# Kernel optimization log

Measured on AMD Instinct MI355X. Metric: run time of the kernel, lower is better.

Reference implementation:

```python
import jax, jax.numpy as jnp
import numpy as np
from math import ceil

CAPACITY_FACTOR = 2.0
MIN_CAPACITY = 4


def setup_inputs() -> dict:
    key = jax.random.key(0)
    ks = jax.random.split(key, 4)
    B, S, D, Di, E = 4, 2048, 1024, 4096, 8
    x = jax.random.normal(ks[0], (B, S, D), dtype=jnp.float32)
    Wr = jax.random.normal(ks[1], (D, E), dtype=jnp.float32) * (D ** -0.5)
    W1 = jax.random.normal(ks[2], (E, D, Di), dtype=jnp.float32) * (D ** -0.5)
    b1 = jnp.zeros((E, Di), dtype=jnp.float32)
    W2 = jax.random.normal(ks[3], (E, Di, D), dtype=jnp.float32) * (Di ** -0.5)
    b2 = jnp.zeros((E, D), dtype=jnp.float32)
    return {"x": x, "Wr": Wr, "W1": W1, "b1": b1, "W2": W2, "b2": b2}


def reference(x, Wr, W1, b1, W2, b2):
    B, S, D = x.shape
    E = Wr.shape[1]
    N = B * S
    k = max(MIN_CAPACITY, ceil(N * CAPACITY_FACTOR / E))  # expert capacity (static)

    xt = x.reshape(N, D)
    scores = jax.nn.softmax(xt @ Wr, axis=-1)          # [N, E] router probs
    G, idx = jax.lax.top_k(scores.T, k)                 # [E, k]: each expert picks top-k tokens

    # dispatch: equivalent to P @ x with P = one_hot(idx, N)
    X_in = xt[idx]                                      # [E, k, D]

    # per-expert MLP (batched over experts): Linear -> GELU(exact) -> Linear
    h = jax.nn.gelu(jnp.einsum('ekd,edh->ekh', X_in, W1) + b1[:, None, :], approximate=False)
    X_e = jnp.einsum('ekh,ehd->ekd', h, W2) + b2[:, None, :]  # [E, k, D]

    # combine: einsum('ijl,ij,ijd->ld', P, G, X_e) == scatter-add of G*X_e at idx
    contrib = (G[..., None] * X_e).reshape(E * k, D)
    out = jnp.zeros((N, D), dtype=x.dtype).at[idx.reshape(-1)].add(contrib)
    return out.reshape(B, S, D)
```

## Files before the change

### kernel.cpp

```cpp
#include <hip/hip_runtime.h>
#include <hip/hip_bf16.h>
#include <cstdint>
#include <cstddef>

#define NTOK 8192
#define DMODEL 1024
#define DFF 4096
#define NEXP 8
#define CAP 2048

typedef __attribute__((ext_vector_type(8))) __bf16 bf16x8;
typedef __attribute__((ext_vector_type(4))) float f32x4;

__device__ __forceinline__ void gload16(const void* g, void* l) {
  __builtin_amdgcn_global_load_lds(
      (__attribute__((address_space(1))) void*)(g),
      (__attribute__((address_space(3))) void*)(l),
      16, 0, 0);
}
#define VMWAIT_(n) asm volatile("s_waitcnt vmcnt(" #n ")" ::: "memory")
#define VMWAIT(n) VMWAIT_(n)
#define MEMFENCE asm volatile("" ::: "memory")

__global__ __launch_bounds__(256) void zero_f32(float* p, int n4) {
  int i = blockIdx.x * blockDim.x + threadIdx.x;
  int stride = gridDim.x * blockDim.x;
  float4 z = make_float4(0.f, 0.f, 0.f, 0.f);
  for (; i < n4; i += stride) ((float4*)p)[i] = z;
}

__global__ __launch_bounds__(256) void router_kernel(
    const float* __restrict__ x, const float* __restrict__ Wr,
    float* __restrict__ scoresT, __hip_bfloat16* __restrict__ xb) {
  const int lane = threadIdx.x & 63;
  const int t = blockIdx.x * 4 + (threadIdx.x >> 6);
  const float* xr = x + (size_t)t * DMODEL;
  float acc[NEXP];
#pragma unroll
  for (int j = 0; j < NEXP; ++j) acc[j] = 0.f;
#pragma unroll
  for (int it = 0; it < DMODEL / 64; ++it) {
    int d = it * 64 + lane;
    float xv = xr[d];
    xb[(size_t)t * DMODEL + d] = __float2bfloat16(xv);
    const float4* w = (const float4*)(Wr + (size_t)d * NEXP);
    float4 w0 = w[0], w1 = w[1];
    acc[0] += xv * w0.x; acc[1] += xv * w0.y; acc[2] += xv * w0.z; acc[3] += xv * w0.w;
    acc[4] += xv * w1.x; acc[5] += xv * w1.y; acc[6] += xv * w1.z; acc[7] += xv * w1.w;
  }
#pragma unroll
  for (int off = 32; off; off >>= 1) {
#pragma unroll
    for (int j = 0; j < NEXP; ++j) acc[j] += __shfl_xor(acc[j], off);
  }
  float m = acc[0];
#pragma unroll
  for (int j = 1; j < NEXP; ++j) m = fmaxf(m, acc[j]);
  float s = 0.f;
#pragma unroll
  for (int j = 0; j < NEXP; ++j) { acc[j] = expf(acc[j] - m); s += acc[j]; }
  float inv = 1.f / s;
  if (lane < NEXP) scoresT[(size_t)lane * NTOK + t] = acc[lane] * inv;
}

__global__ __launch_bounds__(256) void topk_kernel(
    const float* __restrict__ scoresT, float* __restrict__ G, int* __restrict__ IDX) {
  __shared__ uint32_t sb[NTOK];
  __shared__ uint32_t hist[256];
  __shared__ uint32_t s_prefix, s_rem;
  __shared__ uint32_t eq_list[256];
  __shared__ uint32_t eq_cnt, gt_cnt;
  const int e = blockIdx.x, tid = threadIdx.x;
  const float* se = scoresT + (size_t)e * NTOK;
  for (int i = tid; i < NTOK; i += 256) sb[i] = __float_as_uint(se[i]);
  if (tid == 0) { s_prefix = 0u; s_rem = CAP; eq_cnt = 0u; gt_cnt = 0u; }
  __syncthreads();
  for (int r = 0; r < 4; ++r) {
    const int shift = 24 - 8 * r;
    for (int i = tid; i < 256; i += 256) hist[i] = 0u;
    __syncthreads();
    uint32_t pfx = s_prefix;
    for (int i = tid; i < NTOK; i += 256) {
      uint32_t b = sb[i];
      if (((b >> shift) >> 8) == pfx) atomicAdd(&hist[(b >> shift) & 255u], 1u);
    }
    __syncthreads();
    if (tid == 0) {
      uint32_t rem = s_rem, cum = 0u;
      int d = 255;
      for (; d > 0; --d) {
        if (cum + hist[d] >= rem) break;
        cum += hist[d];
      }
      s_prefix = (pfx << 8) | (uint32_t)d;
      s_rem = rem - cum;
    }
    __syncthreads();
  }
  const uint32_t T = s_prefix, need = s_rem;
  for (int i = tid; i < NTOK; i += 256) {
    uint32_t b = sb[i];
    if (b > T) {
      uint32_t p = atomicAdd(&gt_cnt, 1u);
      IDX[(size_t)e * CAP + p] = i;
      G[(size_t)e * CAP + p] = __uint_as_float(b);
    } else if (b == T) {
      uint32_t c = atomicAdd(&eq_cnt, 1u);
      if (c < 256u) eq_list[c] = (uint32_t)i;
    }
  }
  __syncthreads();
  if (tid == 0) {
    uint32_t base = gt_cnt;
    uint32_t c = eq_cnt < 256u ? eq_cnt : 256u;
    for (uint32_t s = 0; s < need; ++s) {
      uint32_t mv = 0xFFFFFFFFu; int mi = 0;
      for (uint32_t j = 0; j < c; ++j)
        if (eq_list[j] < mv) { mv = eq_list[j]; mi = (int)j; }
      eq_list[mi] = 0xFFFFFFFFu;
      IDX[(size_t)e * CAP + base + s] = (int)mv;
      G[(size_t)e * CAP + base + s] = __uint_as_float(T);
    }
  }
}

__global__ __launch_bounds__(256) void transpose_cvt(
    const float* __restrict__ in, __hip_bfloat16* __restrict__ out, int R, int C) {
  __shared__ float tile[32][33];
  const int e = blockIdx.z;
  const float* ine = in + (size_t)e * R * C;
  __hip_bfloat16* oute = out + (size_t)e * R * C;
  const int c0 = blockIdx.x * 32, r0 = blockIdx.y * 32;
  const int tx = threadIdx.x, ty = threadIdx.y;
#pragma unroll
  for (int i = 0; i < 4; ++i)
    tile[ty + i * 8][tx] = ine[(size_t)(r0 + ty + i * 8) * C + (c0 + tx)];
  __syncthreads();
#pragma unroll
  for (int i = 0; i < 4; ++i)
    oute[(size_t)(c0 + ty + i * 8) * R + (r0 + tx)] =
        __float2bfloat16(tile[tx][ty + i * 8]);
}


#define RD_A(BASE, H)                                                          \
  {                                                                            \
    _Pragma("unroll") for (int mi = 0; mi < 4; ++mi)                           \
        _Pragma("unroll") for (int ks = 0; ks < 2; ++ks) av[mi][ks] =          \
        *(const bf16x8*)((BASE) + Ab + offA[(H)*4 + mi][ks]);                  \
  }
#define RD_B(BASE, BV, H2)                                                     \
  {                                                                            \
    _Pragma("unroll") for (int ni = 0; ni < 2; ++ni)                           \
        _Pragma("unroll") for (int ks = 0; ks < 2; ++ks) BV[ni][ks] =          \
        *(const bf16x8*)((BASE) + Bb + offB[(H2)*2 + ni][ks]);                 \
  }
#define STAGE_A(H, BUF)                                                        \
  {                                                                            \
    gload16(pa[(H)*2], (BUF) + (H)*16384 + dst);                               \
    pa[(H)*2] += 128;                                                          \
    gload16(pa[(H)*2 + 1], (BUF) + (H)*16384 + 8192 + dst);                    \
    pa[(H)*2 + 1] += 128;                                                      \
  }
#define STAGE_B(H, BUF)                                                        \
  {                                                                            \
    gload16(pb[(H)*2], (BUF) + 32768 + (H)*16384 + dst);                       \
    pb[(H)*2] += 128;                                                          \
    gload16(pb[(H)*2 + 1], (BUF) + 32768 + (H)*16384 + 8192 + dst);            \
    pb[(H)*2 + 1] += 128;                                                      \
  }
#define PH_PRE                                                                 \
  __builtin_amdgcn_s_barrier();                                                \
  MEMFENCE;                                                                    \
  asm volatile("s_waitcnt lgkmcnt(0)" ::: "memory");                           \
  __builtin_amdgcn_sched_barrier(0);                                           \
  __builtin_amdgcn_s_setprio(1);
#define PH_POST                                                                \
  __builtin_amdgcn_s_setprio(0);                                               \
  __builtin_amdgcn_s_barrier();                                                \
  MEMFENCE;
#define MFMA_Q(MB, NB, BV)                                                     \
  {                                                                            \
    _Pragma("unroll") for (int mi = 0; mi < 4; ++mi)                           \
        _Pragma("unroll") for (int ni = 0; ni < 2; ++ni)                       \
            _Pragma("unroll") for (int ks = 0; ks < 2; ++ks)                   \
                acc[(MB) + mi][(NB) + ni] =                                    \
        __builtin_amdgcn_mfma_f32_16x16x32_bf16(                               \
            av[mi][ks], BV[ni][ks], acc[(MB) + mi][(NB) + ni], 0, 0, 0);       \
  }

template <int NKT>
__device__ __forceinline__ void gemm_core8(
    const char* pa0, const char* pa1, const char* pa2, const char* pa3,
    const char* pb0, const char* pb1, const char* pb2, const char* pb3,
    char* smem, f32x4 (&acc)[8][4]) {
  const int tid = threadIdx.x;
  const int wave = tid >> 6, lane = tid & 63;
  const int wm = wave >> 2, wn = wave & 3;
  const int lrow = lane & 15, lgrp = lane >> 4;
  const int dst = tid * 16;

  const char* pa[4] = {pa0, pa1, pa2, pa3};
  const char* pb[4] = {pb0, pb1, pb2, pb3};

  int offA[8][2], offB[4][2];
#pragma unroll
  for (int mi = 0; mi < 8; ++mi) {
    int rL = mi * 16 + lrow;
#pragma unroll
    for (int ks = 0; ks < 2; ++ks)
      offA[mi][ks] = rL * 128 + ((((ks * 4 + lgrp) + rL) & 7) << 4);
  }
#pragma unroll
  for (int ni = 0; ni < 4; ++ni) {
    int rL = (wn & 1) * 64 + ni * 16 + lrow;
#pragma unroll
    for (int ks = 0; ks < 2; ++ks)
      offB[ni][ks] = rL * 128 + ((((ks * 4 + lgrp) + rL) & 7) << 4);
  }
  const int Ab = wm * 16384;
  const int Bb = 32768 + (wn >> 1) * 16384;

  char* b0 = smem;
  char* b1 = smem + 65536;

#pragma unroll
  for (int g = 0; g < 4; ++g) {
    gload16(pa[g], b0 + (g >> 1) * 16384 + (g & 1) * 8192 + dst);
    pa[g] += 128;
  }
#pragma unroll
  for (int g = 0; g < 4; ++g) {
    gload16(pb[g], b0 + 32768 + (g >> 1) * 16384 + (g & 1) * 8192 + dst);
    pb[g] += 128;
  }
#pragma unroll
  for (int g = 0; g < 4; ++g) {
    gload16(pb[g], b1 + 32768 + (g >> 1) * 16384 + (g & 1) * 8192 + dst);
    pb[g] += 128;
  }
  VMWAIT(4);
  __builtin_amdgcn_s_barrier();
  MEMFENCE;

  bf16x8 av[4][2], bv0[2][2], bv1[2][2];

  for (int i = 0; i < NKT / 2; ++i) {
    const bool st2 = (2 * i + 2 < NKT);
    const bool st3 = (2 * i + 3 < NKT);

    RD_A(b0, 0); RD_B(b0, bv0, 0);
    STAGE_A(0, b1);
    PH_PRE; MFMA_Q(0, 0, bv0); PH_POST;
    RD_B(b0, bv1, 1);
    STAGE_A(1, b1);
    PH_PRE; MFMA_Q(0, 2, bv1); PH_POST;
    RD_A(b0, 1);
    if (st2) STAGE_B(0, b0);
    PH_PRE; MFMA_Q(4, 2, bv1); PH_POST;
    if (st2) STAGE_B(1, b0);
    PH_PRE; MFMA_Q(4, 0, bv0);
    __builtin_amdgcn_s_setprio(0);
    if (st2) { VMWAIT(4); } else { VMWAIT(0); }
    __builtin_amdgcn_s_barrier();
    MEMFENCE;

    RD_A(b1, 0); RD_B(b1, bv0, 0);
    if (st2) STAGE_A(0, b0);
    PH_PRE; MFMA_Q(0, 0, bv0); PH_POST;
    RD_B(b1, bv1, 1);
    if (st2) STAGE_A(1, b0);
    PH_PRE; MFMA_Q(0, 2, bv1); PH_POST;
    RD_A(b1, 1);
    if (st3) STAGE_B(0, b1);
    PH_PRE; MFMA_Q(4, 2, bv1); PH_POST;
    if (st3) STAGE_B(1, b1);
    PH_PRE; MFMA_Q(4, 0, bv0);
    __builtin_amdgcn_s_setprio(0);
    if (st3) { VMWAIT(4); }
    __builtin_amdgcn_s_barrier();
    MEMFENCE;
  }
}

__device__ __forceinline__ float gelu_tanh(float v) {
  float t = 0.7978845608028654f * (v + 0.044715f * v * v * v);
  float e = __expf(2.f * t);
  float th = 1.f - 2.f / (e + 1.f);
  return 0.5f * v * (1.f + th);
}

__global__ __launch_bounds__(512, 2) void gemm1_kernel(
    const __hip_bfloat16* __restrict__ xb,
    const __hip_bfloat16* __restrict__ W1t,
    const float* __restrict__ b1,
    const int* __restrict__ IDX,
    __hip_bfloat16* __restrict__ h, int e0, int nblk) {
  __shared__ __align__(16) char smem[131072];
  int lin = blockIdx.x;
  { int q = nblk >> 3; lin = (lin & 7) * q + (lin >> 3); }
  const int tm = lin & 7, tn = (lin >> 3) & 15, ez = lin >> 7;
  const int e = e0 + ez;
  const int tid = threadIdx.x, wave = tid >> 6, lane = tid & 63;
  const int wm = wave >> 2, wn = wave & 3;
  const int lrow = lane & 15, lgrp = lane >> 4;

  const int r0 = tid >> 3;
  const int ksrc = (((tid & 7) - r0) & 7) * 16;
  const char* pa[4]; const char* pb[4];
#pragma unroll
  for (int g = 0; g < 4; ++g) {
    int m = g * 64 + r0;
    int tok = IDX[e * CAP + tm * 256 + m];
    pa[g] = (const char*)(xb + (size_t)tok * DMODEL) + ksrc;
    int n = g * 64 + r0;
    pb[g] = (const char*)(W1t + ((size_t)e * DFF + tn * 256 + n) * DMODEL) + ksrc;
  }

  f32x4 acc[8][4];
  f32x4 zero = {0.f, 0.f, 0.f, 0.f};
#pragma unroll
  for (int mi = 0; mi < 8; ++mi)
#pragma unroll
    for (int ni = 0; ni < 4; ++ni) acc[mi][ni] = zero;

  gemm_core8<DMODEL / 64>(pa[0], pa[1], pa[2], pa[3],
                          pb[0], pb[1], pb[2], pb[3], smem, acc);

  __hip_bfloat16* he = h + (size_t)ez * CAP * DFF;
  const float* b1e = b1 + (size_t)e * DFF;
  float bvals[4];
#pragma unroll
  for (int ni = 0; ni < 4; ++ni)
    bvals[ni] = b1e[tn * 256 + wn * 64 + ni * 16 + lrow];
#pragma unroll
  for (int mi = 0; mi < 8; ++mi) {
#pragma unroll
    for (int j = 0; j < 4; ++j) {
      int row = tm * 256 + wm * 128 + mi * 16 + lgrp * 4 + j;
      __hip_bfloat16* hrow = he + (size_t)row * DFF;
#pragma unroll
      for (int ni = 0; ni < 4; ++ni) {
        int col = tn * 256 + wn * 64 + ni * 16 + lrow;
        float v = acc[mi][ni][j] + bvals[ni];
        hrow[col] = __float2bfloat16(gelu_tanh(v));
      }
    }
  }
}

__global__ __launch_bounds__(512, 2) void gemm2_kernel(
    const __hip_bfloat16* __restrict__ h,
    const __hip_bfloat16* __restrict__ W2t,
    const float* __restrict__ b2,
    const int* __restrict__ IDX, const float* __restrict__ G,
    float* __restrict__ out, int e0, int nblk) {
  __shared__ __align__(16) char smem[131072];
  int lin = blockIdx.x;
  { int q = nblk >> 3; lin = (lin & 7) * q + (lin >> 3); }
  const int tm = lin & 7, tn = (lin >> 3) & 3, ez = lin >> 5;
  const int e = e0 + ez;
  const int tid = threadIdx.x, wave = tid >> 6, lane = tid & 63;
  const int wm = wave >> 2, wn = wave & 3;
  const int lrow = lane & 15, lgrp = lane >> 4;

  const int r0 = tid >> 3;
  const int ksrc = (((tid & 7) - r0) & 7) * 16;
  const char* pa[4]; const char* pb[4];
#pragma unroll
  for (int g = 0; g < 4; ++g) {
    int m = g * 64 + r0;
    pa[g] = (const char*)(h + ((size_t)ez * CAP + tm * 256 + m) * DFF) + ksrc;
    int n = g * 64 + r0;
    pb[g] = (const char*)(W2t + ((size_t)e * DMODEL + tn * 256 + n) * DFF) + ksrc;
  }

  f32x4 acc[8][4];
  f32x4 zero = {0.f, 0.f, 0.f, 0.f};
#pragma unroll
  for (int mi = 0; mi < 8; ++mi)
#pragma unroll
    for (int ni = 0; ni < 4; ++ni) acc[mi][ni] = zero;

  gemm_core8<DFF / 64>(pa[0], pa[1], pa[2], pa[3],
                       pb[0], pb[1], pb[2], pb[3], smem, acc);

  const float* b2e = b2 + (size_t)e * DMODEL;
  const int* idxe = IDX + (size_t)e * CAP;
  const float* ge = G + (size_t)e * CAP;
  float bvals[4];
#pragma unroll
  for (int ni = 0; ni < 4; ++ni)
    bvals[ni] = b2e[tn * 256 + wn * 64 + ni * 16 + lrow];
#pragma unroll
  for (int mi = 0; mi < 8; ++mi) {
#pragma unroll
    for (int j = 0; j < 4; ++j) {
      int row = tm * 256 + wm * 128 + mi * 16 + lgrp * 4 + j;
      float g = ge[row];
      int tok = idxe[row];
      float* orow = out + (size_t)tok * DMODEL;
#pragma unroll
      for (int ni = 0; ni < 4; ++ni) {
        int col = tn * 256 + wn * 64 + ni * 16 + lrow;
        atomicAdd(orow + col, (acc[mi][ni][j] + bvals[ni]) * g);
      }
    }
  }
}

extern "C" void kernel_launch(void* const* d_in, const int* in_sizes, int n_in,
                              void* d_out, int out_size, void* d_ws, size_t ws_size,
                              hipStream_t stream) {
  const float* x  = (const float*)d_in[0];
  const float* Wr = (const float*)d_in[1];
  const float* W1 = (const float*)d_in[2];
  const float* b1 = (const float*)d_in[3];
  const float* W2 = (const float*)d_in[4];
  const float* b2 = (const float*)d_in[5];
  float* out = (float*)d_out;
  char* ws = (char*)d_ws;

  size_t off = 0;
  float* scoresT = (float*)(ws + off); off += (size_t)NEXP * NTOK * 4;
  float* G       = (float*)(ws + off); off += (size_t)NEXP * CAP * 4;
  int*   IDX     = (int*)(ws + off);   off += (size_t)NEXP * CAP * 4;
  __hip_bfloat16* xb  = (__hip_bfloat16*)(ws + off); off += (size_t)NTOK * DMODEL * 2;
  __hip_bfloat16* W1t = (__hip_bfloat16*)(ws + off); off += (size_t)NEXP * DFF * DMODEL * 2;
  __hip_bfloat16* W2t = (__hip_bfloat16*)(ws + off); off += (size_t)NEXP * DMODEL * DFF * 2;
  __hip_bfloat16* hbuf = (__hip_bfloat16*)(ws + off);
  size_t h_per_e = (size_t)CAP * DFF * 2;
  size_t avail = (ws_size > off) ? (ws_size - off) : 0;
  int EC = (int)(avail / h_per_e);
  if (EC < 1) EC = 1;
  if (EC > NEXP) EC = NEXP;

  zero_f32<<<512, 256, 0, stream>>>(out, out_size / 4);
  router_kernel<<<NTOK / 4, 256, 0, stream>>>(x, Wr, scoresT, xb);
  topk_kernel<<<NEXP, 256, 0, stream>>>(scoresT, G, IDX);
  transpose_cvt<<<dim3(DFF / 32, DMODEL / 32, NEXP), dim3(32, 8), 0, stream>>>(
      W1, W1t, DMODEL, DFF);
  transpose_cvt<<<dim3(DMODEL / 32, DFF / 32, NEXP), dim3(32, 8), 0, stream>>>(
      W2, W2t, DFF, DMODEL);
  for (int e0 = 0; e0 < NEXP; e0 += EC) {
    int ne = (NEXP - e0 < EC) ? (NEXP - e0) : EC;
    int nblk1 = 128 * ne;
    gemm1_kernel<<<nblk1, 512, 0, stream>>>(xb, W1t, b1, IDX, hbuf, e0, nblk1);
    int nblk2 = 32 * ne;
    gemm2_kernel<<<nblk2, 512, 0, stream>>>(hbuf, W2t, b2, IDX, G, out, e0, nblk2);
  }
}
```

Measured before the change: 472.2 us.

## Vectorize stores in transpose and GEMM1 epilogue, drop trailing phase barrier

The weight transpose now writes pairs of bf16 values as 32-bit stores instead of scalar 16-bit stores. The GEMM1 epilogue stages the GELU output tile in swizzled LDS and then writes it out with coalesced 16-byte global stores instead of scattered 2-byte stores. The barrier after each MFMA phase in the pipelined core is removed, leaving only a priority reset. This cuts global store transactions and sync overhead, but removing the barrier risks LDS races if the next stage overwrites buffers that other waves are still reading.

```diff
diff --git a/kernel.cpp b/kernel.cpp
--- a/kernel.cpp
+++ b/kernel.cpp
@@ -136,10 +136,15 @@
   for (int i = 0; i < 4; ++i)
     tile[ty + i * 8][tx] = ine[(size_t)(r0 + ty + i * 8) * C + (c0 + tx)];
   __syncthreads();
-#pragma unroll
-  for (int i = 0; i < 4; ++i)
-    oute[(size_t)(c0 + ty + i * 8) * R + (r0 + tx)] =
-        __float2bfloat16(tile[tx][ty + i * 8]);
+  const int rp = (tx & 15) * 2;
+#pragma unroll
+  for (int i = 0; i < 2; ++i) {
+    int cl = ty + (tx >> 4) * 8 + i * 16;
+    __hip_bfloat16 a = __float2bfloat16(tile[rp][cl]);
+    __hip_bfloat16 b = __float2bfloat16(tile[rp + 1][cl]);
+    ushort2 v = make_ushort2(*(unsigned short*)&a, *(unsigned short*)&b);
+    *(ushort2*)(&oute[(size_t)(c0 + cl) * R + (r0 + rp)]) = v;
+  }
 }
 
 
@@ -175,10 +180,7 @@
   asm volatile("s_waitcnt lgkmcnt(0)" ::: "memory");                           \
   __builtin_amdgcn_sched_barrier(0);                                           \
   __builtin_amdgcn_s_setprio(1);
-#define PH_POST                                                                \
-  __builtin_amdgcn_s_setprio(0);                                               \
-  __builtin_amdgcn_s_barrier();                                                \
-  MEMFENCE;
+#define PH_POST __builtin_amdgcn_s_setprio(0);
 #define MFMA_Q(MB, NB, BV)                                                     \
   {                                                                            \
     _Pragma("unroll") for (int mi = 0; mi < 4; ++mi)                           \
@@ -333,19 +335,33 @@
 #pragma unroll
   for (int ni = 0; ni < 4; ++ni)
     bvals[ni] = b1e[tn * 256 + wn * 64 + ni * 16 + lrow];
+  char* sb = smem;
+  const int wswz = lgrp << 5;
 #pragma unroll
   for (int mi = 0; mi < 8; ++mi) {
 #pragma unroll
     for (int j = 0; j < 4; ++j) {
-      int row = tm * 256 + wm * 128 + mi * 16 + lgrp * 4 + j;
-      __hip_bfloat16* hrow = he + (size_t)row * DFF;
+      int row = wm * 128 + mi * 16 + lgrp * 4 + j;
 #pragma unroll
       for (int ni = 0; ni < 4; ++ni) {
-        int col = tn * 256 + wn * 64 + ni * 16 + lrow;
+        int col = wn * 64 + ni * 16 + lrow;
         float v = acc[mi][ni][j] + bvals[ni];
-        hrow[col] = __float2bfloat16(gelu_tanh(v));
+        v = gelu_tanh(v);
+        *(__hip_bfloat16*)(sb + ((row * 512 + col * 2) ^ wswz)) =
+            __float2bfloat16(v);
       }
     }
+  }
+  __syncthreads();
+  size_t obase = (size_t)(tm * 256) * DFF + tn * 256;
+#pragma unroll
+  for (int c = 0; c < 16; ++c) {
+    int byte = c * 8192 + tid * 16;
+    int row = byte >> 9;
+    int rswz = ((row >> 2) & 3) << 5;
+    bf16x8 vals = *(const bf16x8*)(sb + (byte ^ rswz));
+    int col = (byte & 511) >> 1;
+    *(bf16x8*)(he + obase + (size_t)row * DFF + col) = vals;
   }
 }
 
```

Result: no change. 475.4 us (+0.7%).
